# Optimization experiments

Hardware: AMD Instinct MI355X
Metric: run time of the kernel (lower is better)

The kernel has to match this reference:

```python
import jax, jax.numpy as jnp
import numpy as np

B, L, D = 8, 4096, 1024
MAX_CHUNKS = 128
BOUNDARY_P = 0.03  # ~123 boundaries per sequence, just under max_chunks


def setup_inputs() -> dict:
    key = jax.random.key(0)
    kx, kb = jax.random.split(key)
    x = jax.random.normal(kx, (B, L, D), dtype=jnp.float32)
    # float 'boundary probabilities'; forward thresholds at 0.5 -> produce 0/1 floats
    boundaries = (jax.random.uniform(kb, (B, L)) < BOUNDARY_P).astype(jnp.float32)
    return {"x": x, "boundaries": boundaries}


def reference(x, boundaries):
    """Vectorized equivalent of ChunkLayer.forward.

    Chunk i of a sequence spans [b_i, b_{i+1}) for consecutive boundary
    positions (last chunk runs to seq end). Tokens before the first
    boundary get segment id -1 and are dropped, matching the torch loop.
    Output is mean-pooled chunks, zero-padded/truncated to MAX_CHUNKS.
    """
    Bb, Ll, Dd = x.shape
    bmask = (boundaries > 0.5).astype(jnp.int32)          # [B, L]
    seg = jnp.cumsum(bmask, axis=1) - 1                   # [B, L], -1 before first boundary
    # route dropped (seg<0) and overflow (seg>=MAX_CHUNKS) tokens to a trash segment
    seg = jnp.where((seg < 0) | (seg >= MAX_CHUNKS), MAX_CHUNKS, seg)

    def per_batch(xi, si):
        sums = jax.ops.segment_sum(xi, si, num_segments=MAX_CHUNKS + 1)[:MAX_CHUNKS]       # [C, D]
        cnts = jax.ops.segment_sum(jnp.ones((Ll,), xi.dtype), si,
                                   num_segments=MAX_CHUNKS + 1)[:MAX_CHUNKS]               # [C]
        return sums, cnts

    sums, cnts = jax.vmap(per_batch)(x, seg)              # [B, C, D], [B, C]
    means = jnp.where(cnts[..., None] > 0,
                      sums / jnp.maximum(cnts, 1.0)[..., None],
                      0.0)                                # zero-pad empty chunks
    return means, cnts.astype(jnp.int32)
```

## Files before the change

### kernel.cpp

```cpp
#include <hip/hip_runtime.h>

#define B_DIM 8
#define L_DIM 4096
#define D_DIM 1024
#define MAXC 128
#define RG 4
#define CT 256

__device__ __forceinline__ void f4add(float4& a, const float4& v) {
    a.x += v.x; a.y += v.y; a.z += v.z; a.w += v.w;
}

__global__ void find_boundaries_kernel(const float* __restrict__ bnd,
                                       int* __restrict__ pos,
                                       int* __restrict__ nseg)
{
    const int b = blockIdx.x;
    const int t = threadIdx.x;
    const float* p = bnd + (size_t)b * L_DIM;
    const int base = t * 16;

    unsigned m = 0u;
#pragma unroll
    for (int j = 0; j < 16; ++j) {
        m |= (p[base + j] > 0.5f) ? (1u << j) : 0u;
    }
    int cnt = __popc(m);

    __shared__ int s[256];
    s[t] = cnt;
    __syncthreads();
    for (int off = 1; off < 256; off <<= 1) {
        int v = (t >= off) ? s[t - off] : 0;
        __syncthreads();
        s[t] += v;
        __syncthreads();
    }
    int excl = s[t] - cnt;
    int* op = pos + (size_t)b * L_DIM;
    int idx = excl;
#pragma unroll
    for (int j = 0; j < 16; ++j) {
        if (m & (1u << j)) op[idx++] = base + j;
    }
    if (t == 255) nseg[b] = s[255];
}

__global__ __launch_bounds__(1024)
void pool_chunks_kernel(const float* __restrict__ x,
                        const int* __restrict__ pos,
                        const int* __restrict__ nseg,
                        float* __restrict__ out_means,
                        float* __restrict__ out_cnts)
{
    const int bc = blockIdx.x;
    const int b  = bc >> 7;
    const int c  = bc & (MAXC - 1);
    const int t  = threadIdx.x;
    const int tc = t & (CT - 1);
    const int rg = t >> 8;

    __shared__ float4 red[RG][CT];

    const int n = nseg[b];
    int cnt = 0;

    float4 a0 = make_float4(0.f, 0.f, 0.f, 0.f);
    float4 a1 = a0, a2 = a0, a3 = a0, a4 = a0, a5 = a0, a6 = a0, a7 = a0;

    if (c < n) {
        const int* pp = pos + (size_t)b * L_DIM;
        const int start = pp[c];
        const int end   = (c + 1 < n) ? pp[c + 1] : L_DIM;
        cnt = end - start;

        const int nr = (cnt - rg + RG - 1) / RG;
        const float* xp = x + ((size_t)b * L_DIM + start + rg) * D_DIM + tc * 4;
        const size_t stride = (size_t)RG * D_DIM;

        int k = 0;
        const int rem = nr & 7;
        if (rem & 4) {
            float4 v0 = *reinterpret_cast<const float4*>(xp + (size_t)(k + 0) * stride);
            float4 v1 = *reinterpret_cast<const float4*>(xp + (size_t)(k + 1) * stride);
            float4 v2 = *reinterpret_cast<const float4*>(xp + (size_t)(k + 2) * stride);
            float4 v3 = *reinterpret_cast<const float4*>(xp + (size_t)(k + 3) * stride);
            f4add(a0, v0); f4add(a1, v1); f4add(a2, v2); f4add(a3, v3);
            k += 4;
        }
        if (rem & 2) {
            float4 v0 = *reinterpret_cast<const float4*>(xp + (size_t)(k + 0) * stride);
            float4 v1 = *reinterpret_cast<const float4*>(xp + (size_t)(k + 1) * stride);
            f4add(a4, v0); f4add(a5, v1);
            k += 2;
        }
        if (rem & 1) {
            float4 v0 = *reinterpret_cast<const float4*>(xp + (size_t)k * stride);
            f4add(a6, v0);
            k += 1;
        }
        for (; k + 8 <= nr; k += 8) {
            const float* base = xp + (size_t)k * stride;
            float4 v0 = *reinterpret_cast<const float4*>(base + 0 * stride);
            float4 v1 = *reinterpret_cast<const float4*>(base + 1 * stride);
            float4 v2 = *reinterpret_cast<const float4*>(base + 2 * stride);
            float4 v3 = *reinterpret_cast<const float4*>(base + 3 * stride);
            float4 v4 = *reinterpret_cast<const float4*>(base + 4 * stride);
            float4 v5 = *reinterpret_cast<const float4*>(base + 5 * stride);
            float4 v6 = *reinterpret_cast<const float4*>(base + 6 * stride);
            float4 v7 = *reinterpret_cast<const float4*>(base + 7 * stride);
            f4add(a0, v0); f4add(a1, v1); f4add(a2, v2); f4add(a3, v3);
            f4add(a4, v4); f4add(a5, v5); f4add(a6, v6); f4add(a7, v7);
        }
        f4add(a0, a1); f4add(a2, a3); f4add(a4, a5); f4add(a6, a7);
        f4add(a0, a2); f4add(a4, a6);
        f4add(a0, a4);
    }

    red[rg][tc] = a0;
    __syncthreads();

    if (t < CT) {
        float4 s0 = red[0][t];
        f4add(s0, red[1][t]);
        f4add(s0, red[2][t]);
        f4add(s0, red[3][t]);
        const float inv = (cnt > 0) ? (1.0f / (float)cnt) : 0.0f;
        s0.x *= inv; s0.y *= inv; s0.z *= inv; s0.w *= inv;
        float4* op = reinterpret_cast<float4*>(out_means + (size_t)bc * D_DIM) + t;
        *op = s0;
        if (t == 0) out_cnts[bc] = (float)cnt;
    }
}

extern "C" void kernel_launch(void* const* d_in, const int* in_sizes, int n_in,
                              void* d_out, int out_size, void* d_ws, size_t ws_size,
                              hipStream_t stream)
{
    const float* x   = (const float*)d_in[0];
    const float* bnd = (const float*)d_in[1];

    float* out = (float*)d_out;
    float* out_means = out;
    float* out_cnts  = out + (size_t)B_DIM * MAXC * D_DIM;

    int* pos  = (int*)d_ws;
    int* nseg = pos + (size_t)B_DIM * L_DIM;

    find_boundaries_kernel<<<B_DIM, 256, 0, stream>>>(bnd, pos, nseg);
    pool_chunks_kernel<<<B_DIM * MAXC, 1024, 0, stream>>>(x, pos, nseg,
                                                          out_means, out_cnts);
}
```

Measured before the change: 34.45 us.

## Fuse boundary scan into pooling kernel, recompute chunk bounds per block

```diff
diff --git a/kernel.cpp b/kernel.cpp
--- a/kernel.cpp
+++ b/kernel.cpp
@@ -11,45 +11,9 @@
     a.x += v.x; a.y += v.y; a.z += v.z; a.w += v.w;
 }
 
-__global__ void find_boundaries_kernel(const float* __restrict__ bnd,
-                                       int* __restrict__ pos,
-                                       int* __restrict__ nseg)
-{
-    const int b = blockIdx.x;
-    const int t = threadIdx.x;
-    const float* p = bnd + (size_t)b * L_DIM;
-    const int base = t * 16;
-
-    unsigned m = 0u;
-#pragma unroll
-    for (int j = 0; j < 16; ++j) {
-        m |= (p[base + j] > 0.5f) ? (1u << j) : 0u;
-    }
-    int cnt = __popc(m);
-
-    __shared__ int s[256];
-    s[t] = cnt;
-    __syncthreads();
-    for (int off = 1; off < 256; off <<= 1) {
-        int v = (t >= off) ? s[t - off] : 0;
-        __syncthreads();
-        s[t] += v;
-        __syncthreads();
-    }
-    int excl = s[t] - cnt;
-    int* op = pos + (size_t)b * L_DIM;
-    int idx = excl;
-#pragma unroll
-    for (int j = 0; j < 16; ++j) {
-        if (m & (1u << j)) op[idx++] = base + j;
-    }
-    if (t == 255) nseg[b] = s[255];
-}
-
 __global__ __launch_bounds__(1024)
-void pool_chunks_kernel(const float* __restrict__ x,
-                        const int* __restrict__ pos,
-                        const int* __restrict__ nseg,
+void fused_chunk_kernel(const float* __restrict__ x,
+                        const float* __restrict__ bnd,
                         float* __restrict__ out_means,
                         float* __restrict__ out_cnts)
 {
@@ -60,18 +24,57 @@
     const int tc = t & (CT - 1);
     const int rg = t >> 8;
 
+    __shared__ int s[256];
+    __shared__ int sb[2];
     __shared__ float4 red[RG][CT];
 
-    const int n = nseg[b];
+    if (t == 0) { sb[0] = 0; sb[1] = L_DIM; }
+
+    unsigned m = 0u;
+    int cnt16 = 0;
+    if (t < 256) {
+        const float* p = bnd + (size_t)b * L_DIM + t * 16;
+        const float4* p4 = reinterpret_cast<const float4*>(p);
+#pragma unroll
+        for (int q = 0; q < 4; ++q) {
+            float4 v = p4[q];
+            if (v.x > 0.5f) m |= 1u << (q * 4 + 0);
+            if (v.y > 0.5f) m |= 1u << (q * 4 + 1);
+            if (v.z > 0.5f) m |= 1u << (q * 4 + 2);
+            if (v.w > 0.5f) m |= 1u << (q * 4 + 3);
+        }
+        cnt16 = __popc(m);
+        s[t] = cnt16;
+    }
+    __syncthreads();
+    for (int off = 1; off < 256; off <<= 1) {
+        int v = (t >= off && t < 256) ? s[t - off] : 0;
+        __syncthreads();
+        if (t < 256) s[t] += v;
+        __syncthreads();
+    }
+    const int n = s[255];
+    if (t < 256 && m != 0u) {
+        int idx = s[t] - cnt16;
+        const int base = t * 16;
+#pragma unroll
+        for (int j = 0; j < 16; ++j) {
+            if (m & (1u << j)) {
+                if (idx == c)     sb[0] = base + j;
+                if (idx == c + 1) sb[1] = base + j;
+                ++idx;
+            }
+        }
+    }
+    __syncthreads();
+
     int cnt = 0;
-
     float4 a0 = make_float4(0.f, 0.f, 0.f, 0.f);
     float4 a1 = a0, a2 = a0, a3 = a0, a4 = a0, a5 = a0, a6 = a0, a7 = a0;
 
     if (c < n) {
-        const int* pp = pos + (size_t)b * L_DIM;
-        const int start = pp[c];
-        const int end   = (c + 1 < n) ? pp[c + 1] : L_DIM;
+        const int start = sb[0];
+        const int end   = sb[1];
         cnt = end - start;
 
         const int nr = (cnt - rg + RG - 1) / RG;
@@ -144,10 +147,6 @@
     float* out_means = out;
     float* out_cnts  = out + (size_t)B_DIM * MAXC * D_DIM;
 
-    int* pos  = (int*)d_ws;
-    int* nseg = pos + (size_t)B_DIM * L_DIM;
-
-    find_boundaries_kernel<<<B_DIM, 256, 0, stream>>>(bnd, pos, nseg);
-    pool_chunks_kernel<<<B_DIM * MAXC, 1024, 0, stream>>>(x, pos, nseg,
+    fused_chunk_kernel<<<B_DIM * MAXC, 1024, 0, stream>>>(x, bnd,
                                                           out_means, out_cnts);
 }
```

After: 31.82 us. 7.6% less time.
